# Kernel optimization log

Hardware: AMD Instinct MI355X
Metric: run time of the kernel (lower is better)

Reference implementation:

```python
import jax, jax.numpy as jnp
import numpy as np

DX = 0.1
DY = 0.1
W_B = 1000.0
W_PARALLEL = 1000.0
W_DIV = 100.0
EPS = 1e-10


def setup_inputs() -> dict:
    key = jax.random.key(0)
    k1, k2 = jax.random.split(key)
    outputs = jax.random.normal(k1, (2, 3, 256, 256, 64), dtype=jnp.float32)
    targets = jax.random.normal(k2, (2, 4, 256, 256, 64), dtype=jnp.float32)
    return {"outputs": outputs, "targets": targets}


def _corners(f):
    # 8 shifted views f[..., i:, j:, k:] (with 0 -> [0:-1], 1 -> [1:]) on dims 2,3,4
    s0, s1 = slice(0, -1), slice(1, None)
    return {(i, j, k): f[:, :, (s1 if i else s0), (s1 if j else s0), (s1 if k else s0)]
            for i in (0, 1) for j in (0, 1) for k in (0, 1)}


def _forward(outputs, targets):
    bx_p, by_p, bz_p = outputs[:, 0:1], outputs[:, 1:2], outputs[:, 2:3]
    bx_t, by_t, bz_t = targets[:, 0:1], targets[:, 1:2], targets[:, 2:3]

    loss_b = (jnp.mean((bx_p**2 + by_p**2 - bx_t**2 - by_t**2) ** 2 / (bx_t**2 + by_t**2 + EPS))
              + jnp.mean((bz_p - bz_t) ** 4 / (bz_t**2 + EPS)))
    loss_parallel = jnp.mean((bx_p * by_t - by_p * bx_t) ** 2
                             / (bx_t**2 + by_t**2 + bz_t**2 + EPS))

    bx = _corners(bx_p)
    by = _corners(by_p)
    bz = _corners(bz_p)
    z = _corners(targets[:, 3:4])

    num = (0.25 * (bx[1, 0, 0] + bx[1, 1, 0] + bx[1, 0, 1] + bx[1, 1, 1]) * DY * 0.5 * (z[1, 0, 1] - z[1, 0, 0] + z[1, 1, 1] - z[1, 1, 0])
           - 0.25 * (bx[0, 0, 0] + bx[0, 1, 0] + bx[0, 0, 1] + bx[0, 1, 1]) * DY * 0.5 * (z[0, 0, 1] - z[0, 0, 0] + z[0, 1, 1] - z[0, 1, 0])
           + 0.25 * (by[0, 1, 0] + by[1, 1, 0] + by[0, 1, 1] + by[1, 1, 1]) * DX * 0.5 * (z[0, 1, 1] - z[0, 1, 0] + z[1, 1, 1] - z[1, 1, 0])
           - 0.25 * (by[0, 0, 0] + by[1, 0, 0] + by[0, 0, 1] + by[1, 0, 1]) * DX * 0.5 * (z[0, 0, 1] - z[0, 0, 0] + z[1, 0, 1] - z[1, 0, 0])
           + 0.25 * (bz[0, 0, 1] + bz[0, 1, 1] + bz[1, 0, 1] + bz[1, 1, 1]) * DX * DY
           - 0.25 * (bz[0, 0, 0] + bz[0, 1, 0] + bz[1, 0, 0] + bz[1, 1, 0]) * DX * DY
           + (bx[0, 0, 1] + bx[1, 0, 1] + bx[1, 1, 1]) * DY * (z[0, 0, 1] - z[1, 0, 1]) / 6
           + (bx[0, 1, 1] + bx[1, 1, 1] + bx[1, 0, 1]) * DY * (z[0, 1, 1] - z[1, 1, 1]) / 6
           + (by[1, 0, 1] + by[1, 1, 1] + by[0, 1, 1]) * DX * (z[1, 0, 1] - z[1, 1, 1]) / 6
           + (by[0, 0, 1] + by[0, 1, 1] + by[1, 1, 1]) * DX * (z[0, 0, 1] - z[0, 1, 1]) / 6
           - (bx[0, 0, 0] + bx[1, 0, 0] + bx[1, 1, 0]) * DY * (z[0, 0, 0] - z[1, 0, 0]) / 6
           - (bx[0, 1, 0] + bx[1, 1, 0] + bx[1, 0, 0]) * DY * (z[0, 1, 0] - z[1, 1, 0]) / 6
           - (by[1, 0, 0] + by[1, 1, 0] + by[0, 1, 0]) * DX * (z[1, 0, 0] - z[1, 1, 0]) / 6
           - (by[0, 0, 0] + by[0, 1, 0] + by[1, 1, 0]) * DX * (z[0, 0, 0] - z[0, 1, 0]) / 6)

    bx_c = sum(bx[c] for c in sorted(bx)) * 0.125
    by_c = sum(by[c] for c in sorted(by)) * 0.125
    bz_c = sum(bz[c] for c in sorted(bz)) * 0.125
    den = bx_c**2 + by_c**2 + bz_c**2 + EPS

    loss_div = jnp.mean(num**2 / den) / DX**2 / DY**2

    return (W_B * loss_b + W_PARALLEL * loss_parallel, W_DIV * loss_div)


def reference(outputs, targets):
    return _forward(outputs, targets)
```

## Files before the change

### kernel.cpp

```cpp
#include <hip/hip_runtime.h>

constexpr int B = 2, X = 256, Y = 256, Z = 64;
constexpr int CO = X * Y * Z;
constexpr int YZ = Y * Z;
constexpr long long N_PTS   = (long long)B * X * Y * Z;
constexpr long long M_CELLS = (long long)B * (X-1) * (Y-1) * (Z-1);

constexpr int ROWS = 4;
constexpr int SEGS = Y / ROWS;
constexpr int TPB  = 256;
constexpr int WPB  = TPB / 64;
constexpr int NSEG   = B * SEGS * X;
constexpr int BLOCKS = NSEG / WPB;

#define EPSc 1e-10f
#define SIXTH (1.0f / 6.0f)
#define RCPF(v) __builtin_amdgcn_rcpf(v)

#define F4C(v, c) (((c) == 0) ? (v).x : ((c) == 1) ? (v).y : ((c) == 2) ? (v).z : (v).w)

__global__ __launch_bounds__(TPB, 4) void loss_main(const float* __restrict__ outs,
                                                    const float* __restrict__ tgts,
                                                    double* __restrict__ partial) {
    const int lane = threadIdx.x & 63;
    const int wv   = threadIdx.x >> 6;
    const int seg  = blockIdx.x * WPB + wv;

    const int b  = seg >> 14;
    const int r  = seg & 16383;
    const int sy = r >> 8;
    const int x  = r & 255;
    const int y0 = sy * ROWS;

    const int row = lane >> 4;
    const int zi  = (lane & 15) << 2;
    const int y_own = y0 + row;
    const int y_up  = (y_own + 1 < Y) ? (y_own + 1) : (Y - 1);
    const int x_up  = (x + 1 < X) ? (x + 1) : (X - 1);
    const bool xvalid = (x < X - 1);
    const bool yvalid = (y_own < Y - 1);

    const float* ob = outs + (size_t)b * 3 * CO;
    const float* tb = tgts + (size_t)b * 4 * CO;
    const int off00 = x    * YZ + y_own * Z + zi;
    const int off01 = x    * YZ + y_up  * Z + zi;
    const int off10 = x_up * YZ + y_own * Z + zi;
    const int off11 = x_up * YZ + y_up  * Z + zi;

    #define LD4(p, off) (*(const float4*)((p) + (off)))

    const float4 obx   = LD4(ob, 0 * CO + off00);
    const float4 oby   = LD4(ob, 1 * CO + off00);
    const float4 obz   = LD4(ob, 2 * CO + off00);
    const float4 tbx   = LD4(tb, 0 * CO + off00);
    const float4 tby   = LD4(tb, 1 * CO + off00);
    const float4 tbz   = LD4(tb, 2 * CO + off00);
    const float4 tzc   = LD4(tb, 3 * CO + off00);
    const float4 obx1  = LD4(ob, 0 * CO + off10);
    const float4 oby1  = LD4(ob, 1 * CO + off10);
    const float4 obz1  = LD4(ob, 2 * CO + off10);
    const float4 tzc1  = LD4(tb, 3 * CO + off10);
    const float4 obxy  = LD4(ob, 0 * CO + off01);
    const float4 obyy  = LD4(ob, 1 * CO + off01);
    const float4 obzy  = LD4(ob, 2 * CO + off01);
    const float4 tzcy  = LD4(tb, 3 * CO + off01);
    const float4 obxy1 = LD4(ob, 0 * CO + off11);
    const float4 obyy1 = LD4(ob, 1 * CO + off11);
    const float4 obzy1 = LD4(ob, 2 * CO + off11);
    const float4 tzcy1 = LD4(tb, 3 * CO + off11);

    double s_pt = 0.0;
    double s_dv = 0.0;

    {
        float pt4 = 0.0f;
        #pragma unroll
        for (int c = 0; c < 4; ++c) {
            const float bxp = F4C(obx, c), byp = F4C(oby, c), bzp = F4C(obz, c);
            const float bxt = F4C(tbx, c), byt = F4C(tby, c), bzt = F4C(tbz, c);
            const float bxt2 = bxt * bxt, byt2 = byt * byt, bzt2 = bzt * bzt;
            const float dxy = bxt2 + byt2;
            const float t1 = bxp * bxp + byp * byp - dxy;
            const float e1 = t1 * t1 * RCPF(dxy + EPSc);
            const float dd = bzp - bzt;
            const float dd2 = dd * dd;
            const float e2 = dd2 * dd2 * RCPF(bzt2 + EPSc);
            const float cr = bxp * byt - byp * bxt;
            const float e3 = cr * cr * RCPF(dxy + bzt2 + EPSc);
            pt4 += e1 + e2 + e3;
        }
        s_pt += (double)pt4;
    }

    if (xvalid) {
        float sxp[5], sxm[5], syp[5], sym[5];
        float zxp[5], zxm[5], zyp[5], zym[5];
        float Sx[5], Sy[5], Sz[5], G2[5];

        #pragma unroll
        for (int t = 0; t < 4; ++t) {
            const float bx00 = F4C(obx, t),   bx10 = F4C(obx1, t);
            const float bx01 = F4C(obxy, t),  bx11 = F4C(obxy1, t);
            const float by00 = F4C(oby, t),   by10 = F4C(oby1, t);
            const float by01 = F4C(obyy, t),  by11 = F4C(obyy1, t);
            const float bz00 = F4C(obz, t),   bz10 = F4C(obz1, t);
            const float bz01 = F4C(obzy, t),  bz11 = F4C(obzy1, t);
            const float zc00 = F4C(tzc, t),   zc10 = F4C(tzc1, t);
            const float zc01 = F4C(tzcy, t),  zc11 = F4C(tzcy1, t);

            sxp[t] = bx10 + bx11;   sxm[t] = bx00 + bx01;
            syp[t] = by01 + by11;   sym[t] = by00 + by10;
            zxp[t] = zc10 + zc11;   zxm[t] = zc00 + zc01;
            zyp[t] = zc01 + zc11;   zym[t] = zc00 + zc10;
            Sx[t] = sxp[t] + sxm[t];
            Sy[t] = syp[t] + sym[t];
            Sz[t] = (bz00 + bz01) + (bz10 + bz11);
            G2[t] = 0.025f * Sz[t]
                  + SIXTH * ((bx00 + sxp[t]) * (zc00 - zc10)
                           + (bx01 + sxp[t]) * (zc01 - zc11)
                           + (by10 + syp[t]) * (zc10 - zc11)
                           + (by00 + syp[t]) * (zc00 - zc01));
        }
        sxp[4] = __shfl_down(sxp[0], 1);
        sxm[4] = __shfl_down(sxm[0], 1);
        syp[4] = __shfl_down(syp[0], 1);
        sym[4] = __shfl_down(sym[0], 1);
        zxp[4] = __shfl_down(zxp[0], 1);
        zxm[4] = __shfl_down(zxm[0], 1);
        zyp[4] = __shfl_down(zyp[0], 1);
        zym[4] = __shfl_down(zym[0], 1);
        Sz[4]  = __shfl_down(Sz[0],  1);
        G2[4]  = __shfl_down(G2[0],  1);
        Sx[4] = sxp[4] + sxm[4];
        Sy[4] = syp[4] + sym[4];

        float dv4 = 0.0f;
        #pragma unroll
        for (int c = 0; c < 4; ++c) {
            const float fx = (sxp[c] + sxp[c+1]) * (zxp[c+1] - zxp[c])
                           - (sxm[c] + sxm[c+1]) * (zxm[c+1] - zxm[c])
                           + (syp[c] + syp[c+1]) * (zyp[c+1] - zyp[c])
                           - (sym[c] + sym[c+1]) * (zym[c+1] - zym[c]);
            const float num2 = 0.125f * fx + (G2[c+1] - G2[c]);
            const float SxS = Sx[c] + Sx[c+1];
            const float SyS = Sy[c] + Sy[c+1];
            const float SzS = Sz[c] + Sz[c+1];
            const float q = SxS * SxS + SyS * SyS + SzS * SzS;
            const float den = 0.015625f * q + EPSc;
            const float v = num2 * num2 * RCPF(den);
            const bool ok = yvalid && ((zi + c) < Z - 1);
            dv4 += ok ? v : 0.0f;
        }
        s_dv += (double)dv4;
    }

    for (int off = 32; off > 0; off >>= 1) {
        s_pt += __shfl_down(s_pt, off);
        s_dv += __shfl_down(s_dv, off);
    }

    __shared__ double lds_pt[WPB];
    __shared__ double lds_dv[WPB];
    if (lane == 0) { lds_pt[wv] = s_pt; lds_dv[wv] = s_dv; }
    __syncthreads();
    if (threadIdx.x == 0) {
        double p = 0.0, d = 0.0;
        #pragma unroll
        for (int w = 0; w < WPB; ++w) { p += lds_pt[w]; d += lds_dv[w]; }
        partial[2 * blockIdx.x]     = p;
        partial[2 * blockIdx.x + 1] = d;
    }
}

__global__ __launch_bounds__(256) void loss_finalize(const double* __restrict__ partial,
                                                     float* __restrict__ out) {
    double s0 = 0.0, s1 = 0.0;
    for (int i = threadIdx.x; i < BLOCKS; i += 256) {
        s0 += partial[2 * i];
        s1 += partial[2 * i + 1];
    }
    const int lane = threadIdx.x & 63;
    const int wave = threadIdx.x >> 6;
    for (int off = 32; off > 0; off >>= 1) {
        s0 += __shfl_down(s0, off);
        s1 += __shfl_down(s1, off);
    }
    __shared__ double l0[4], l1[4];
    if (lane == 0) { l0[wave] = s0; l1[wave] = s1; }
    __syncthreads();
    if (threadIdx.x == 0) {
        double p = 0.0, d = 0.0;
        #pragma unroll
        for (int w = 0; w < 4; ++w) { p += l0[w]; d += l1[w]; }
        const double out0 = 1000.0 * (p / (double)N_PTS);
        const double out1 = 10000.0 * (d / (double)M_CELLS);
        out[0] = (float)out0;
        out[1] = (float)out1;
    }
}

extern "C" void kernel_launch(void* const* d_in, const int* in_sizes, int n_in,
                              void* d_out, int out_size, void* d_ws, size_t ws_size,
                              hipStream_t stream) {
    const float* outs = (const float*)d_in[0];
    const float* tgts = (const float*)d_in[1];
    float* out = (float*)d_out;
    double* partial = (double*)d_ws;

    loss_main<<<BLOCKS, TPB, 0, stream>>>(outs, tgts, partial);
    loss_finalize<<<1, 256, 0, stream>>>(partial, out);
}
```

Measured before the change: 264.2 us.

## Stage block tile in LDS via global_load_lds to share y-neighbor rows

Each block now covers 16 y-rows of one x column pair and loads the 8 channel planes (3 outputs plus z target, for x and x+1) directly into LDS with global_load_lds, plus a halo row. Threads then read their own and next-row float4 values from LDS instead of issuing separate global loads for the y+1 neighbor, cutting redundant global/L2 traffic. Target bx/by/bz are read with nontemporal loads. This adds a block-wide barrier and about 36KB of LDS per block, which may limit occupancy.

```diff
diff --git a/kernel.cpp b/kernel.cpp
--- a/kernel.cpp
+++ b/kernel.cpp
@@ -1,4 +1,5 @@
 #include <hip/hip_runtime.h>
+#include <stdint.h>
 
 constexpr int B = 2, X = 256, Y = 256, Z = 64;
 constexpr int CO = X * Y * Z;
@@ -6,68 +7,96 @@
 constexpr long long N_PTS   = (long long)B * X * Y * Z;
 constexpr long long M_CELLS = (long long)B * (X-1) * (Y-1) * (Z-1);
 
-constexpr int ROWS = 4;
-constexpr int SEGS = Y / ROWS;
-constexpr int TPB  = 256;
-constexpr int WPB  = TPB / 64;
-constexpr int NSEG   = B * SEGS * X;
-constexpr int BLOCKS = NSEG / WPB;
+constexpr int RPB = 16;
+constexpr int TPB = 256;
+constexpr int WPB = TPB / 64;
+constexpr int BLOCKS = B * (Y / RPB) * X;
+
+constexpr int SSTRIDE = 1152;
 
 #define EPSc 1e-10f
 #define SIXTH (1.0f / 6.0f)
 #define RCPF(v) __builtin_amdgcn_rcpf(v)
 
+typedef float fvec4 __attribute__((ext_vector_type(4)));
+
 #define F4C(v, c) (((c) == 0) ? (v).x : ((c) == 1) ? (v).y : ((c) == 2) ? (v).z : (v).w)
+
+typedef const __attribute__((address_space(1))) uint32_t* gptr_t;
+typedef __attribute__((address_space(3))) uint32_t* lptr_t;
 
 __global__ __launch_bounds__(TPB, 4) void loss_main(const float* __restrict__ outs,
                                                     const float* __restrict__ tgts,
                                                     double* __restrict__ partial) {
+    __shared__ float sm[8 * SSTRIDE];
+
     const int lane = threadIdx.x & 63;
     const int wv   = threadIdx.x >> 6;
-    const int seg  = blockIdx.x * WPB + wv;
-
-    const int b  = seg >> 14;
-    const int r  = seg & 16383;
+    const int blk  = blockIdx.x;
+
+    const int b  = blk >> 12;
+    const int r  = blk & 4095;
     const int sy = r >> 8;
     const int x  = r & 255;
-    const int y0 = sy * ROWS;
-
-    const int row = lane >> 4;
-    const int zi  = (lane & 15) << 2;
-    const int y_own = y0 + row;
-    const int y_up  = (y_own + 1 < Y) ? (y_own + 1) : (Y - 1);
-    const int x_up  = (x + 1 < X) ? (x + 1) : (X - 1);
+    const int y0 = sy * RPB;
+    const int xc1 = (x + 1 < X) ? (x + 1) : (X - 1);
     const bool xvalid = (x < X - 1);
-    const bool yvalid = (y_own < Y - 1);
 
     const float* ob = outs + (size_t)b * 3 * CO;
     const float* tb = tgts + (size_t)b * 4 * CO;
-    const int off00 = x    * YZ + y_own * Z + zi;
-    const int off01 = x    * YZ + y_up  * Z + zi;
-    const int off10 = x_up * YZ + y_own * Z + zi;
-    const int off11 = x_up * YZ + y_up  * Z + zi;
-
-    #define LD4(p, off) (*(const float4*)((p) + (off)))
-
-    const float4 obx   = LD4(ob, 0 * CO + off00);
-    const float4 oby   = LD4(ob, 1 * CO + off00);
-    const float4 obz   = LD4(ob, 2 * CO + off00);
-    const float4 tbx   = LD4(tb, 0 * CO + off00);
-    const float4 tby   = LD4(tb, 1 * CO + off00);
-    const float4 tbz   = LD4(tb, 2 * CO + off00);
-    const float4 tzc   = LD4(tb, 3 * CO + off00);
-    const float4 obx1  = LD4(ob, 0 * CO + off10);
-    const float4 oby1  = LD4(ob, 1 * CO + off10);
-    const float4 obz1  = LD4(ob, 2 * CO + off10);
-    const float4 tzc1  = LD4(tb, 3 * CO + off10);
-    const float4 obxy  = LD4(ob, 0 * CO + off01);
-    const float4 obyy  = LD4(ob, 1 * CO + off01);
-    const float4 obzy  = LD4(ob, 2 * CO + off01);
-    const float4 tzcy  = LD4(tb, 3 * CO + off01);
-    const float4 obxy1 = LD4(ob, 0 * CO + off11);
-    const float4 obyy1 = LD4(ob, 1 * CO + off11);
-    const float4 obzy1 = LD4(ob, 2 * CO + off11);
-    const float4 tzcy1 = LD4(tb, 3 * CO + off11);
+
+    const int row_l = wv * 4 + (lane >> 4);
+    const int zi    = (lane & 15) << 2;
+    const int y_own = y0 + row_l;
+    const bool yvalid = (y_own < Y - 1);
+
+    const float* tb0 = tb + (size_t)x * YZ + (size_t)y_own * Z + zi;
+    const fvec4 tbx = __builtin_nontemporal_load((const fvec4*)(tb0 + 0 * CO));
+    const fvec4 tby = __builtin_nontemporal_load((const fvec4*)(tb0 + 1 * CO));
+    const fvec4 tbz = __builtin_nontemporal_load((const fvec4*)(tb0 + 2 * CO));
+
+    const int y16 = (y0 + 16 < Y) ? (y0 + 16) : (Y - 1);
+    #pragma unroll
+    for (int j = 0; j < 2; ++j) {
+        const int s   = wv * 2 + j;
+        const int col = s >> 2;
+        const int ch  = s & 3;
+        const int xs  = col ? xc1 : x;
+        const float* gbase = (ch < 3 ? ob + (size_t)ch * CO : tb + (size_t)3 * CO)
+                           + (size_t)xs * YZ;
+        const float* gsrc  = gbase + (size_t)y0 * Z;
+        float* ldst = sm + s * SSTRIDE;
+        #pragma unroll
+        for (int k = 0; k < 4; ++k) {
+            __builtin_amdgcn_global_load_lds((gptr_t)(gsrc + k * 256 + lane * 4),
+                                             (lptr_t)(ldst + k * 256 + lane * 4),
+                                             16, 0, 0);
+        }
+        const float* gsrc16 = gbase + (size_t)y16 * Z;
+        __builtin_amdgcn_global_load_lds((gptr_t)(gsrc16 + lane),
+                                         (lptr_t)(ldst + 16 * 64 + lane),
+                                         4, 0, 0);
+    }
+    __syncthreads();
+
+    #define SMF4(col, ch, row) (*(const fvec4*)(sm + ((col) * 4 + (ch)) * SSTRIDE + (row) * 64 + zi))
+
+    const fvec4 obx   = SMF4(0, 0, row_l);
+    const fvec4 oby   = SMF4(0, 1, row_l);
+    const fvec4 obz   = SMF4(0, 2, row_l);
+    const fvec4 tzc   = SMF4(0, 3, row_l);
+    const fvec4 obx1  = SMF4(1, 0, row_l);
+    const fvec4 oby1  = SMF4(1, 1, row_l);
+    const fvec4 obz1  = SMF4(1, 2, row_l);
+    const fvec4 tzc1  = SMF4(1, 3, row_l);
+    const fvec4 obxy  = SMF4(0, 0, row_l + 1);
+    const fvec4 obyy  = SMF4(0, 1, row_l + 1);
+    const fvec4 obzy  = SMF4(0, 2, row_l + 1);
+    const fvec4 tzcy  = SMF4(0, 3, row_l + 1);
+    const fvec4 obxy1 = SMF4(1, 0, row_l + 1);
+    const fvec4 obyy1 = SMF4(1, 1, row_l + 1);
+    const fvec4 obzy1 = SMF4(1, 2, row_l + 1);
+    const fvec4 tzcy1 = SMF4(1, 3, row_l + 1);
 
     double s_pt = 0.0;
     double s_dv = 0.0;
```

Measured after the change: 253.9 us. 1.04x faster.
